# Kernel optimization log

Measured on AMD Instinct MI355X. Metric: run time of the kernel, lower is better.

The kernel has to match this reference:

```python
import jax, jax.numpy as jnp
import numpy as np

NF = 128                 # num_filters
C_STATE = NF * 3 // 2    # ODE state channels (output of conv_up_embed_1) = 192
EPS = 1e-5               # InstanceNorm2d eps
N_STEPS = 4              # fixed-step RK4 steps over t in [0, 1]
DT = 1.0 / N_STEPS

nl = jax.nn.softplus     # get_nonlinearity('softplus')


def instance_norm(x):
    # InstanceNorm2d(affine=False): normalize over (H, W) per (N, C)
    m = x.mean(axis=(2, 3), keepdims=True)
    v = x.var(axis=(2, 3), keepdims=True)
    return (x - m) * jax.lax.rsqrt(v + EPS)


def conv2d(x, w, b):
    y = jax.lax.conv_general_dilated(
        x, w, window_strides=(1, 1), padding='SAME',
        dimension_numbers=('NCHW', 'OIHW', 'NCHW'))
    return y + b[None, :, None, None]


def setup_inputs() -> dict:
    key = jax.random.key(0)
    ks = jax.random.split(key, 10)
    B, H, W = 4, 64, 64
    s = 0.05
    return {
        'x':    jax.random.normal(ks[0], (B, NF, H, W), jnp.float32),
        'skip': jax.random.normal(ks[1], (B, NF, 2 * H, 2 * W), jnp.float32),
        # InitialVelocity: 3x3 conv nf -> nf
        'iv_w': jax.random.normal(ks[2], (NF, NF, 3, 3), jnp.float32) * s,
        'iv_b': jax.random.normal(ks[3], (NF,), jnp.float32) * s,
        # conv_up_embed_1: 1x1 conv 3nf -> 3nf//2
        'up_w': jax.random.normal(ks[4], (C_STATE, 3 * NF, 1, 1), jnp.float32) * s,
        'up_b': jax.random.normal(ks[5], (C_STATE,), jnp.float32) * s,
        # ConvSODEFunc convs (second-order: dv/dt = f(z, v))
        'f1_w': jax.random.normal(ks[6], (C_STATE // 2, C_STATE, 3, 3), jnp.float32) * s,
        'f1_b': jax.random.normal(ks[7], (C_STATE // 2,), jnp.float32) * s,
        'f2_w': jax.random.normal(ks[8], (C_STATE // 2, C_STATE // 2, 3, 3), jnp.float32) * s,
        'f2_b': jax.random.normal(ks[9], (C_STATE // 2,), jnp.float32) * s,
    }


def _ode_f(y, f1_w, f1_b, f2_w, f2_b):
    # second-order ODE: state y = [z, v]; dz/dt = v, dv/dt = f(y)
    c = y.shape[1] // 2
    v = y[:, c:]
    u = nl(conv2d(instance_norm(y), f1_w, f1_b))   # [B, C/2, H, W]
    dv = nl(conv2d(instance_norm(u), f2_w, f2_b))  # [B, C/2, H, W]
    return jnp.concatenate([v, dv], axis=1)


def reference(x, skip, iv_w, iv_b, up_w, up_b, f1_w, f1_b, f2_w, f2_b):
    # InitialVelocity (counter == 0): concat learned velocity -> 2*nf channels
    v0 = nl(conv2d(instance_norm(x), iv_w, iv_b))
    y = jnp.concatenate([x, v0], axis=1)                       # [B, 2nf, H, W]
    B, C, H, W = y.shape
    # bilinear upsample x2, align_corners=False (half-pixel centers)
    y = jax.image.resize(y, (B, C, 2 * H, 2 * W), method='bilinear')
    y = jnp.concatenate([y, skip], axis=1)                     # [B, 3nf, 2H, 2W]
    y = nl(conv2d(y, up_w, up_b))                              # [B, 3nf//2, 2H, 2W]
    # ODEBlock: integrate t: 0 -> 1, fixed-step RK4 via lax.scan
    f = lambda s: _ode_f(s, f1_w, f1_b, f2_w, f2_b)

    def step(s, _):
        k1 = f(s)
        k2 = f(s + 0.5 * DT * k1)
        k3 = f(s + 0.5 * DT * k2)
        k4 = f(s + DT * k3)
        s = s + (DT / 6.0) * (k1 + 2.0 * k2 + 2.0 * k3 + k4)
        return s, None

    y, _ = jax.lax.scan(step, y, None, length=N_STEPS)
    return y
```

## Files before the change

### kernel.cpp

```cpp
#include <hip/hip_runtime.h>
#include <math.h>

#define BB 4
#define NF 128
#define CS 192
#define CH 96
#define H1 64
#define W1 64
#define H2 128
#define W2 128
#define P1 (H1*W1)
#define P2 (H2*W2)
#define EPSV 1e-5f
#define DTV 0.25f
#define NSLICE 32
#define SLOTSZ (1536 * NSLICE)

typedef __attribute__((ext_vector_type(8))) short short8;
typedef __attribute__((ext_vector_type(4))) float f32x4;

__device__ __forceinline__ float softplus_f(float x) {
    return fmaxf(x, 0.0f) + __logf(1.0f + __expf(-fabsf(x)));
}
__device__ __forceinline__ unsigned f2bf(float f) {
    unsigned u = __float_as_uint(f);
    return (u + 0x7FFFu + ((u >> 16) & 1u)) >> 16;
}
__device__ __forceinline__ float bf2f(short s) {
    return __uint_as_float(((unsigned)(unsigned short)s) << 16);
}
__device__ __forceinline__ int packbf(float a, float b) {
    return (int)(f2bf(a) | (f2bf(b) << 16));
}

__global__ __launch_bounds__(256) void zero_kernel(float* __restrict__ p, int n) {
    int i = blockIdx.x * 256 + threadIdx.x;
    if (i < n) p[i] = 0.f;
}

__global__ __launch_bounds__(256) void meanvar_raw_kernel(const float* __restrict__ x,
                                                          float* __restrict__ mv, int HW) {
    int bc = blockIdx.x;
    const float* p = x + (size_t)bc * HW;
    float s = 0.f, s2 = 0.f;
    for (int i = threadIdx.x; i < HW; i += 256) {
        float v = p[i];
        s += v; s2 += v * v;
    }
    __shared__ float sh[512];
    sh[threadIdx.x] = s; sh[256 + threadIdx.x] = s2;
    __syncthreads();
    for (int o = 128; o > 0; o >>= 1) {
        if (threadIdx.x < o) {
            sh[threadIdx.x] += sh[threadIdx.x + o];
            sh[256 + threadIdx.x] += sh[256 + threadIdx.x + o];
        }
        __syncthreads();
    }
    if (threadIdx.x == 0) {
        mv[2 * bc]     = sh[0];
        mv[2 * bc + 1] = sh[256];
    }
}

__global__ __launch_bounds__(256) void repack_w_kernel(const float* __restrict__ w,
                                                       short* __restrict__ wq,
                                                       int Cout, int Cin) {
    int idx = blockIdx.x * 256 + threadIdx.x;
    int total = Cout * Cin * 9;
    if (idx >= total) return;
    int tap = idx % 9;
    int t = idx / 9;
    int ci = t % Cin, co = t / Cin;
    int NITl = Cin >> 5, COGl = Cout >> 4;
    int cog = co >> 4, lx = co & 15;
    int it = ci >> 5, q = (ci >> 3) & 3, e = ci & 7;
    size_t o = ((((size_t)tap * NITl + it) * COGl + cog) * 64 + q * 16 + lx) * 8 + e;
    wq[o] = (short)f2bf(w[idx]);
}

__global__ __launch_bounds__(256) void repack_w1_kernel(const float* __restrict__ w,
                                                        short* __restrict__ wq, int n) {
    int i = blockIdx.x * 256 + threadIdx.x;
    if (i < n) wq[i] = (short)f2bf(w[i]);
}

__global__ __launch_bounds__(256) void xcvt_kernel(const float* __restrict__ x,
                                                   short* __restrict__ xbf) {
    __shared__ int buf[64 * 68];
    const int tid = threadIdx.x;
    const int px = tid & 63, jj = tid >> 6;
    const int px0 = blockIdx.x * 64;
    const int b = blockIdx.y;
#pragma unroll
    for (int ji = 0; ji < 16; ji++) {
        int j = jj + 4 * ji;
        int c = 2 * j;
        float a = x[((size_t)(b * NF + c)) * P1 + px0 + px];
        float d = x[((size_t)(b * NF + c + 1)) * P1 + px0 + px];
        buf[px * 68 + j] = packbf(a, d);
    }
    __syncthreads();
#pragma unroll
    for (int k = 0; k < 4; k++) {
        int idx = tid + 256 * k;
        int p2 = idx >> 4, w4 = idx & 15;
        int4 v = *(const int4*)&buf[p2 * 68 + w4 * 4];
        *(int4*)(xbf + ((size_t)b * P1 + px0 + p2) * NF + w4 * 8) = v;
    }
}

template<int CIN, int NCG, bool OUTBF, bool SUMS>
__global__ __launch_bounds__(512) void conv3x3_mfma(
    const short* __restrict__ in, const float* __restrict__ mvsums,
    const short* __restrict__ wq, const float* __restrict__ bias,
    float* __restrict__ outf, short* __restrict__ outbf, float* __restrict__ osum,
    int CoutT, int H, int W, int outC, int outCoff, int coblk)
{
    constexpr int ROWS = CIN + 8;
    constexpr int STGI = 180 * ROWS / 2;
    constexpr int SMEMI = (OUTBF && 128 * 52 > STGI) ? 128 * 52 : STGI;
    constexpr int NCGH = NCG / 2;
    __shared__ int smem[SMEMI];
    short* xt = (short*)smem;
    __shared__ float mvm[CIN], mvr[CIN];
    __shared__ float shs[2 * CH];
    const int tid = threadIdx.x;
    const int w8 = tid >> 6, lane = tid & 63;
    const int wy = w8 & 3, wc = w8 >> 2;
    const int lx = lane & 15, q = lane >> 4;
    const int x0 = blockIdx.x * 16, y0 = blockIdx.y * 8;
    const int b = blockIdx.z / coblk;
    const int co_base = (blockIdx.z % coblk) * (NCG * 16);
    const int slice = (blockIdx.x + (blockIdx.y << 3)) & (NSLICE - 1);
    const int HWp = H * W;
    const short* inb = in + (size_t)b * HWp * CIN;

    const float invHW = 1.0f / (float)HWp;
    for (int c = tid; c < CIN; c += 512) {
        float s = 0.f, s2 = 0.f;
#pragma unroll
        for (int sl = 0; sl < NSLICE; sl++) {
            s  += mvsums[(size_t)sl * 1536 + (b * CIN + c) * 2];
            s2 += mvsums[(size_t)sl * 1536 + (b * CIN + c) * 2 + 1];
        }
        float m  = s * invHW;
        float var = fmaxf(s2 * invHW - m * m, 0.f);
        mvm[c] = m;
        mvr[c] = rsqrtf(var + EPSV);
    }
    if (SUMS) for (int c = tid; c < 2 * CH; c += 512) shs[c] = 0.f;
    __syncthreads();

    constexpr int PARTS = CIN / 8;
    constexpr int TOT = 180 * PARTS;
    constexpr int NJ = (TOT + 511) / 512;
#pragma unroll
    for (int k = 0; k < NJ; k++) {
        int j = tid + 512 * k;
        if (j < TOT) {
            int px = j / PARTS, part = j - px * PARTS;
            int yy = px / 18, xx = px - yy * 18;
            int gy = y0 + yy - 1, gx = x0 + xx - 1;
            int4 wv = make_int4(0, 0, 0, 0);
            if (gy >= 0 && gy < H && gx >= 0 && gx < W) {
                int cb = part * 8;
                short8 v = *(const short8*)(inb + (size_t)(gy * W + gx) * CIN + cb);
                float4 m0 = *(const float4*)&mvm[cb];
                float4 m1 = *(const float4*)&mvm[cb + 4];
                float4 r0 = *(const float4*)&mvr[cb];
                float4 r1 = *(const float4*)&mvr[cb + 4];
                wv.x = packbf((bf2f(v[0]) - m0.x) * r0.x, (bf2f(v[1]) - m0.y) * r0.y);
                wv.y = packbf((bf2f(v[2]) - m0.z) * r0.z, (bf2f(v[3]) - m0.w) * r0.w);
                wv.z = packbf((bf2f(v[4]) - m1.x) * r1.x, (bf2f(v[5]) - m1.y) * r1.y);
                wv.w = packbf((bf2f(v[6]) - m1.z) * r1.z, (bf2f(v[7]) - m1.w) * r1.w);
            }
            *(int4*)(&xt[px * ROWS + part * 8]) = wv;
        }
    }
    __syncthreads();

    f32x4 acc[2][NCGH];
#pragma unroll
    for (int rr = 0; rr < 2; rr++)
#pragma unroll
        for (int cg = 0; cg < NCGH; cg++) acc[rr][cg] = (f32x4)(0.f);

    constexpr int NIT = CIN / 32;
    const int COGl = CoutT >> 4;
    const short* wbase = wq + ((size_t)((co_base >> 4) + wc * NCGH) * 64 + lane) * 8;
#pragma unroll 2
    for (int it = 0; it < NIT; it++) {
#pragma unroll
        for (int tap = 0; tap < 9; tap++) {
            const int dy = tap / 3, dx = tap % 3;
            const int slot0 = (tap * NIT + it) * COGl;
            short8 a[NCGH];
#pragma unroll
            for (int cg = 0; cg < NCGH; cg++)
                a[cg] = *(const short8*)(wbase + (size_t)(slot0 + cg) * 512);
#pragma unroll
            for (int rr = 0; rr < 2; rr++) {
                int row = wy * 2 + rr;
                short8 bfr = *(const short8*)(
                    &xt[((row + dy) * 18 + lx + dx) * ROWS + it * 32 + q * 8]);
#pragma unroll
                for (int cg = 0; cg < NCGH; cg++)
                    acc[rr][cg] = __builtin_amdgcn_mfma_f32_16x16x32_bf16(
                        a[cg], bfr, acc[rr][cg], 0, 0, 0);
            }
        }
    }

    if (OUTBF) __syncthreads();

    float s1l[NCGH][4], s2l[NCGH][4];
    if (SUMS) {
#pragma unroll
        for (int cg = 0; cg < NCGH; cg++)
#pragma unroll
            for (int r = 0; r < 4; r++) { s1l[cg][r] = 0.f; s2l[cg][r] = 0.f; }
    }
#pragma unroll
    for (int rr = 0; rr < 2; rr++) {
        int y = y0 + wy * 2 + rr;
#pragma unroll
        for (int cg = 0; cg < NCGH; cg++) {
            float v[4];
#pragma unroll
            for (int r = 0; r < 4; r++) {
                int co = wc * (NCGH * 16) + cg * 16 + q * 4 + r;
                v[r] = softplus_f(acc[rr][cg][r] + bias[co_base + co]);
                if (SUMS) { s1l[cg][r] += v[r]; s2l[cg][r] += v[r] * v[r]; }
            }
            if (OUTBF) {
                int pl = (wy * 2 + rr) * 16 + lx;
                smem[pl * 52 + wc * (NCGH * 8) + cg * 8 + q * 2]     = packbf(v[0], v[1]);
                smem[pl * 52 + wc * (NCGH * 8) + cg * 8 + q * 2 + 1] = packbf(v[2], v[3]);
            } else {
                float* ob = outf + ((size_t)b * outC + outCoff + co_base) * HWp
                            + y * W + x0 + lx;
#pragma unroll
                for (int r = 0; r < 4; r++)
                    ob[(size_t)(wc * (NCGH * 16) + cg * 16 + q * 4 + r) * HWp] = v[r];
            }
        }
    }
    if (OUTBF) {
        __syncthreads();
#pragma unroll
        for (int k = 0; k < 3; k++) {
            int idx = tid + 512 * k;
            int pl2 = idx / 12, w4 = idx % 12;
            int4 v = *(const int4*)&smem[pl2 * 52 + w4 * 4];
            int pix = (y0 + (pl2 >> 4)) * W + x0 + (pl2 & 15);
            *(int4*)(outbf + ((size_t)b * HWp + pix) * 96 + w4 * 8) = v;
        }
    }
    if (SUMS) {
#pragma unroll
        for (int cg = 0; cg < NCGH; cg++)
#pragma unroll
            for (int r = 0; r < 4; r++) {
                float a1 = s1l[cg][r], a2 = s2l[cg][r];
#pragma unroll
                for (int mask = 1; mask < 16; mask <<= 1) {
                    a1 += __shfl_xor(a1, mask);
                    a2 += __shfl_xor(a2, mask);
                }
                if (lx == 0) {
                    int co = wc * (NCGH * 16) + cg * 16 + q * 4 + r;
                    atomicAdd(&shs[2 * co], a1);
                    atomicAdd(&shs[2 * co + 1], a2);
                }
            }
        __syncthreads();
        for (int c = tid; c < 2 * NCG * 16; c += 512)
            atomicAdd(&osum[(size_t)slice * 1536 + (size_t)b * 2 * NCG * 16 + c], shs[c]);
    }
}

__global__ __launch_bounds__(256) void upsample_kernel(
    const float* __restrict__ x, const float* __restrict__ v0,
    const float* __restrict__ skip, short* __restrict__ ycat)
{
    __shared__ int buf[64 * 196];
    const int tid = threadIdx.x;
    const int px = tid & 63, jj = tid >> 6;
    const int px0 = blockIdx.x * 64;
    const int b = blockIdx.y;
    const int pxg = px0 + px;
    const int ox = pxg & 127, oy = pxg >> 7;
    int my = oy >> 1, mx = ox >> 1;
    int iy0 = (oy & 1) ? my : my - 1;
    float wy0 = (oy & 1) ? 0.75f : 0.25f;
    int ix0 = (ox & 1) ? mx : mx - 1;
    float wx0 = (ox & 1) ? 0.75f : 0.25f;
    int iy1 = min(iy0 + 1, H1 - 1); iy0 = max(iy0, 0);
    int ix1 = min(ix0 + 1, W1 - 1); ix0 = max(ix0, 0);
    float wy1 = 1.f - wy0, wx1 = 1.f - wx0;
    float w00 = wy0 * wx0, w01 = wy0 * wx1, w10 = wy1 * wx0, w11 = wy1 * wx1;
    int o00 = iy0 * W1 + ix0, o01 = iy0 * W1 + ix1;
    int o10 = iy1 * W1 + ix0, o11 = iy1 * W1 + ix1;
#pragma unroll 4
    for (int ji = 0; ji < 48; ji++) {
        int j = jj + 4 * ji;
        int c = 2 * j;
        float a, d;
        if (c < 256) {
            const float* s0 = (c < 128) ? x + ((size_t)(b * NF + c)) * P1
                                        : v0 + ((size_t)(b * NF + c - 128)) * P1;
            const float* s1 = s0 + P1;
            a = w00 * s0[o00] + w01 * s0[o01] + w10 * s0[o10] + w11 * s0[o11];
            d = w00 * s1[o00] + w01 * s1[o01] + w10 * s1[o10] + w11 * s1[o11];
        } else {
            const float* sk = skip + ((size_t)(b * NF + c - 256)) * P2 + pxg;
            a = sk[0]; d = sk[P2];
        }
        buf[px * 196 + j] = packbf(a, d);
    }
    __syncthreads();
#pragma unroll
    for (int k = 0; k < 12; k++) {
        int idx = tid + 256 * k;
        int p2 = idx / 48, w4 = idx % 48;
        int4 v = *(const int4*)&buf[p2 * 196 + w4 * 4];
        *(int4*)(ycat + ((size_t)b * P2 + px0 + p2) * 384 + w4 * 8) = v;
    }
}

__global__ __launch_bounds__(256) void conv1x1_mfma(
    const short* __restrict__ ycat, const short* __restrict__ wq,
    const float* __restrict__ bias, float* __restrict__ out,
    short* __restrict__ sbf, float* __restrict__ osum)
{
    __shared__ int smem[64 * 100];
    short* xs = (short*)smem;
    const int tid = threadIdx.x;
    const int wave = tid >> 6, lane = tid & 63;
    const int lx = lane & 15, q = lane >> 4;
    const int p0 = blockIdx.x * 64;
    const int b = blockIdx.y;
    const int slice = blockIdx.x & (NSLICE - 1);
    const int spx = tid >> 2, spart = tid & 3;
    const size_t gofs = ((size_t)b * P2 + p0 + spx) * 384 + spart * 8;
    const int ldso = spx * 40 + spart * 8;

    f32x4 acc[3][4];
#pragma unroll
    for (int cg = 0; cg < 3; cg++)
#pragma unroll
        for (int pg = 0; pg < 4; pg++) acc[cg][pg] = (f32x4)(0.f);

    short8 pf = *(const short8*)(ycat + gofs);
    for (int it = 0; it < 12; it++) {
        if (it > 0) __syncthreads();
        *(short8*)(&xs[ldso]) = pf;
        __syncthreads();
        if (it < 11) pf = *(const short8*)(ycat + gofs + (it + 1) * 32);
        const short* wl = wq + (size_t)(wave * 48 + lx) * 384 + it * 32 + q * 8;
        short8 a[3];
#pragma unroll
        for (int cg = 0; cg < 3; cg++)
            a[cg] = *(const short8*)(wl + (size_t)cg * 16 * 384);
#pragma unroll
        for (int pg = 0; pg < 4; pg++) {
            short8 bfr = *(const short8*)(&xs[(pg * 16 + lx) * 40 + q * 8]);
#pragma unroll
            for (int cg = 0; cg < 3; cg++)
                acc[cg][pg] = __builtin_amdgcn_mfma_f32_16x16x32_bf16(
                    a[cg], bfr, acc[cg][pg], 0, 0, 0);
        }
    }
    __syncthreads();

    float s1a[3][4], s2a[3][4];
#pragma unroll
    for (int cg = 0; cg < 3; cg++)
#pragma unroll
        for (int r = 0; r < 4; r++) { s1a[cg][r] = 0.f; s2a[cg][r] = 0.f; }
#pragma unroll
    for (int cg = 0; cg < 3; cg++) {
        int co0 = wave * 48 + cg * 16 + q * 4;
#pragma unroll
        for (int pg = 0; pg < 4; pg++) {
            int pl = pg * 16 + lx;
            float v[4];
#pragma unroll
            for (int r = 0; r < 4; r++) {
                v[r] = softplus_f(acc[cg][pg][r] + bias[co0 + r]);
                out[((size_t)(b * CS + co0 + r)) * P2 + p0 + pl] = v[r];
                s1a[cg][r] += v[r]; s2a[cg][r] += v[r] * v[r];
            }
            smem[pl * 100 + (co0 >> 1)]     = packbf(v[0], v[1]);
            smem[pl * 100 + (co0 >> 1) + 1] = packbf(v[2], v[3]);
        }
    }
    __syncthreads();
#pragma unroll
    for (int k = 0; k < 6; k++) {
        int idx = tid + 256 * k;
        int p2 = idx / 24, w4 = idx % 24;
        int4 v = *(const int4*)&smem[p2 * 100 + w4 * 4];
        *(int4*)(sbf + ((size_t)b * P2 + p0 + p2) * 192 + w4 * 8) = v;
    }
#pragma unroll
    for (int cg = 0; cg < 3; cg++)
#pragma unroll
        for (int r = 0; r < 4; r++) {
            float a1 = s1a[cg][r], a2 = s2a[cg][r];
#pragma unroll
            for (int mask = 1; mask < 16; mask <<= 1) {
                a1 += __shfl_xor(a1, mask);
                a2 += __shfl_xor(a2, mask);
            }
            if (lx == 0) {
                int co = wave * 48 + cg * 16 + q * 4 + r;
                atomicAdd(&osum[(size_t)slice * 1536 + ((size_t)b * CS + co) * 2], a1);
                atomicAdd(&osum[(size_t)slice * 1536 + ((size_t)b * CS + co) * 2 + 1], a2);
            }
        }
}

__global__ __launch_bounds__(256) void combine_kernel(
    const float* __restrict__ S, const float* __restrict__ Gx,
    const float* __restrict__ Gp, short* __restrict__ T, float* __restrict__ osum,
    float ca1, float ca2, float cb)
{
    __shared__ int buf[64 * 100];
    const int tid = threadIdx.x;
    const int px = tid & 63, jj = tid >> 6;
    const int px0 = blockIdx.x * 64;
    const int b = blockIdx.y;
    const int pxg = px0 + px;
    const int slice = blockIdx.x & (NSLICE - 1);
#pragma unroll 3
    for (int ji = 0; ji < 12; ji++) {
        int j = jj + 4 * ji;
        int c = 2 * j;
        size_t ia = ((size_t)(b * CS + c)) * P2 + pxg;
        size_t ib = ia + (size_t)CH * P2;
        size_t ig = ((size_t)(b * CH + c)) * P2 + pxg;
        float sa0 = S[ia], sa1 = S[ia + P2];
        float sb0 = S[ib], sb1 = S[ib + P2];
        float gx0 = Gx[ig], gx1 = Gx[ig + P2];
        float gp0 = Gp[ig], gp1 = Gp[ig + P2];
        buf[px * 100 + j]      = packbf(sa0 + ca1 * sb0 + ca2 * gx0,
                                        sa1 + ca1 * sb1 + ca2 * gx1);
        buf[px * 100 + 48 + j] = packbf(sb0 + cb * gp0, sb1 + cb * gp1);
    }
    __syncthreads();
#pragma unroll
    for (int k = 0; k < 6; k++) {
        int idx = tid + 256 * k;
        int p2 = idx / 24, w4 = idx % 24;
        int4 v = *(const int4*)&buf[p2 * 100 + w4 * 4];
        *(int4*)(T + ((size_t)b * P2 + px0 + p2) * 192 + w4 * 8) = v;
    }
    if (tid < 192) {
        int jj2 = tid >> 1, s = tid & 1;
        float s1lo = 0.f, s2lo = 0.f, s1hi = 0.f, s2hi = 0.f;
#pragma unroll 8
        for (int p = s; p < 64; p += 2) {
            int v = buf[p * 100 + jj2];
            float lo = bf2f((short)v), hi = bf2f((short)(v >> 16));
            s1lo += lo; s2lo += lo * lo; s1hi += hi; s2hi += hi * hi;
        }
        s1lo += __shfl_xor(s1lo, 1); s2lo += __shfl_xor(s2lo, 1);
        s1hi += __shfl_xor(s1hi, 1); s2hi += __shfl_xor(s2hi, 1);
        if (s == 0) {
            int c = 2 * jj2;
            float* dst = &osum[(size_t)slice * 1536 + ((size_t)b * CS + c) * 2];
            atomicAdd(dst, s1lo);
            atomicAdd(dst + 1, s2lo);
            atomicAdd(dst + 2, s1hi);
            atomicAdd(dst + 3, s2hi);
        }
    }
}

template<bool SBF>
__global__ __launch_bounds__(256) void final_kernel(
    float* __restrict__ S, const float* __restrict__ G1, const float* __restrict__ G2,
    const float* __restrict__ G3, const float* __restrict__ G4,
    short* __restrict__ sbf, float* __restrict__ osum)
{
    __shared__ int buf[SBF ? 64 * 100 : 4];
    const int tid = threadIdx.x;
    const int px = tid & 63, jj = tid >> 6;
    const int px0 = blockIdx.x * 64;
    const int b = blockIdx.y;
    const int pxg = px0 + px;
    const int slice = blockIdx.x & (NSLICE - 1);
    const float cA = DTV * DTV / 6.0f, cB = DTV / 6.0f;
#pragma unroll 3
    for (int ji = 0; ji < 12; ji++) {
        int j = jj + 4 * ji;
        int c = 2 * j;
        size_t ia = ((size_t)(b * CS + c)) * P2 + pxg;
        size_t ib = ia + (size_t)CH * P2;
        size_t ig = ((size_t)(b * CH + c)) * P2 + pxg;
        float sa0 = S[ia], sa1 = S[ia + P2];
        float sb0 = S[ib], sb1 = S[ib + P2];
        float g10 = G1[ig], g11 = G1[ig + P2];
        float g20 = G2[ig], g21 = G2[ig + P2];
        float g30 = G3[ig], g31 = G3[ig + P2];
        float g40 = G4[ig], g41 = G4[ig + P2];
        float na0 = sa0 + DTV * sb0 + cA * (g10 + g20 + g30);
        float na1 = sa1 + DTV * sb1 + cA * (g11 + g21 + g31);
        float nb0 = sb0 + cB * (g10 + 2.f * g20 + 2.f * g30 + g40);
        float nb1 = sb1 + cB * (g11 + 2.f * g21 + 2.f * g31 + g41);
        S[ia] = na0; S[ia + P2] = na1;
        S[ib] = nb0; S[ib + P2] = nb1;
        if (SBF) {
            buf[px * 100 + j]      = packbf(na0, na1);
            buf[px * 100 + 48 + j] = packbf(nb0, nb1);
        }
    }
    if (SBF) {
        __syncthreads();
#pragma unroll
        for (int k = 0; k < 6; k++) {
            int idx = tid + 256 * k;
            int p2 = idx / 24, w4 = idx % 24;
            int4 v = *(const int4*)&buf[p2 * 100 + w4 * 4];
            *(int4*)(sbf + ((size_t)b * P2 + px0 + p2) * 192 + w4 * 8) = v;
        }
        if (tid < 192) {
            int jj2 = tid >> 1, s = tid & 1;
            float s1lo = 0.f, s2lo = 0.f, s1hi = 0.f, s2hi = 0.f;
#pragma unroll 8
            for (int p = s; p < 64; p += 2) {
                int v = buf[p * 100 + jj2];
                float lo = bf2f((short)v), hi = bf2f((short)(v >> 16));
                s1lo += lo; s2lo += lo * lo; s1hi += hi; s2hi += hi * hi;
            }
            s1lo += __shfl_xor(s1lo, 1); s2lo += __shfl_xor(s2lo, 1);
            s1hi += __shfl_xor(s1hi, 1); s2hi += __shfl_xor(s2hi, 1);
            if (s == 0) {
                int c = 2 * jj2;
                float* dst = &osum[(size_t)slice * 1536 + ((size_t)b * CS + c) * 2];
                atomicAdd(dst, s1lo);
                atomicAdd(dst + 1, s2lo);
                atomicAdd(dst + 2, s1hi);
                atomicAdd(dst + 3, s2hi);
            }
        }
    }
}

extern "C" void kernel_launch(void* const* d_in, const int* in_sizes, int n_in,
                              void* d_out, int out_size, void* d_ws, size_t ws_size,
                              hipStream_t stream) {
    (void)in_sizes; (void)n_in; (void)out_size; (void)ws_size;
    const float* x    = (const float*)d_in[0];
    const float* skip = (const float*)d_in[1];
    const float* iv_w = (const float*)d_in[2];
    const float* iv_b = (const float*)d_in[3];
    const float* up_w = (const float*)d_in[4];
    const float* up_b = (const float*)d_in[5];
    const float* f1_w = (const float*)d_in[6];
    const float* f1_b = (const float*)d_in[7];
    const float* f2_w = (const float*)d_in[8];
    const float* f2_b = (const float*)d_in[9];

    float* S = (float*)d_out;
    float* ws = (float*)d_ws;
    const size_t NGf = (size_t)BB * CH * P2;
    float* G1 = ws;
    float* G2 = G1 + NGf;
    float* G3 = G2 + NGf;
    float* G4 = G3 + NGf;
    short* T   = (short*)(G4 + NGf);
    short* U   = T + (size_t)BB * P2 * CS;
    short* SBF = U + (size_t)BB * P2 * CH;
    float* MVS = (float*)(SBF + (size_t)BB * P2 * CS);
    short* IVQ = (short*)(MVS + (size_t)34 * SLOTSZ);
    short* F1Q = IVQ + (size_t)9 * NF * NF;
    short* F2Q = F1Q + (size_t)9 * CH * CS;
    short* UPQ = F2Q + (size_t)9 * CH * CH;
    short* YCAT = (short*)G1;
    float* V0   = G3;
    short* XBF  = (short*)G4;

    auto slot = [&](int i) { return MVS + (size_t)i * SLOTSZ; };

    zero_kernel<<<(34 * SLOTSZ + 255) / 256, 256, 0, stream>>>(MVS, 34 * SLOTSZ);
    repack_w_kernel<<<(NF * NF * 9 + 255) / 256, 256, 0, stream>>>(iv_w, IVQ, NF, NF);
    repack_w_kernel<<<(CH * CS * 9 + 255) / 256, 256, 0, stream>>>(f1_w, F1Q, CH, CS);
    repack_w_kernel<<<(CH * CH * 9 + 255) / 256, 256, 0, stream>>>(f2_w, F2Q, CH, CH);
    repack_w1_kernel<<<(CS * 384 + 255) / 256, 256, 0, stream>>>(up_w, UPQ, CS * 384);

    meanvar_raw_kernel<<<BB * NF, 256, 0, stream>>>(x, slot(0), P1);
    xcvt_kernel<<<dim3(P1 / 64, BB), 256, 0, stream>>>(x, XBF);
    conv3x3_mfma<128, 4, false, false><<<dim3(W1 / 16, H1 / 8, BB * 2), 512, 0, stream>>>(
        XBF, slot(0), IVQ, iv_b, V0, nullptr, nullptr, NF, H1, W1, NF, 0, 2);
    upsample_kernel<<<dim3(P2 / 64, BB), 256, 0, stream>>>(x, V0, skip, YCAT);
    conv1x1_mfma<<<dim3(P2 / 64, BB), 256, 0, stream>>>(YCAT, UPQ, up_b, S, SBF, slot(1));

    const float h = DTV;
    float* G[4] = {G1, G2, G3, G4};
    int sc = 2;
    float* yslot = slot(1);
    const dim3 egrd(P2 / 64, BB);

    for (int step = 0; step < 4; step++) {
        for (int sub = 0; sub < 4; sub++) {
            const short* Ybf = (sub == 0) ? SBF : T;
            float* uslot = slot(sc++);
            conv3x3_mfma<192, 6, true, true><<<dim3(W2 / 16, H2 / 8, BB), 512, 0, stream>>>(
                Ybf, yslot, F1Q, f1_b, nullptr, U, uslot, CH, H2, W2, CH, 0, 1);
            conv3x3_mfma<96, 6, false, false><<<dim3(W2 / 16, H2 / 8, BB), 512, 0, stream>>>(
                U, uslot, F2Q, f2_b, G[sub], nullptr, nullptr, CH, H2, W2, CH, 0, 1);
            if (sub < 3) {
                float ca1, ca2, cb;
                const float *Gx, *Gp;
                if (sub == 0)      { ca1 = h/2; ca2 = 0.f;     Gx = G1; Gp = G1; cb = h/2; }
                else if (sub == 1) { ca1 = h/2; ca2 = h*h/4;   Gx = G1; Gp = G2; cb = h/2; }
                else               { ca1 = h;   ca2 = h*h/2;   Gx = G2; Gp = G3; cb = h;   }
                float* tslot = slot(sc++);
                combine_kernel<<<egrd, 256, 0, stream>>>(S, Gx, Gp, T, tslot, ca1, ca2, cb);
                yslot = tslot;
            }
        }
        if (step < 3) {
            float* sslot = slot(sc++);
            final_kernel<true><<<egrd, 256, 0, stream>>>(S, G1, G2, G3, G4, SBF, sslot);
            yslot = sslot;
        } else {
            final_kernel<false><<<egrd, 256, 0, stream>>>(S, G1, G2, G3, G4, SBF, nullptr);
        }
    }
}
```

Baseline: 1.628 ms.

## Halve conv3x3 block to 4 waves with 4 rows each; stage full 1x1 input tile

The 3x3 conv kernel now runs 256 threads (4 waves) instead of 512. Each wave computes four output rows instead of two, so every weight fragment loaded from global memory feeds twice as many MFMAs. The 1x1 up-projection kernel now loads the whole 64-pixel by 384-channel tile into LDS once, replacing twelve synchronized chunk loads. Its weights are repacked into the MFMA fragment layout so each lane can read them contiguously. In exchange there are more accumulator registers per wave, fewer waves per block to hide latency, and larger LDS use in the 1x1 kernel.

```diff
diff --git a/kernel.cpp b/kernel.cpp
--- a/kernel.cpp
+++ b/kernel.cpp
@@ -80,9 +80,16 @@
 }
 
 __global__ __launch_bounds__(256) void repack_w1_kernel(const float* __restrict__ w,
-                                                        short* __restrict__ wq, int n) {
-    int i = blockIdx.x * 256 + threadIdx.x;
-    if (i < n) wq[i] = (short)f2bf(w[i]);
+                                                        short* __restrict__ wq,
+                                                        int Cout, int Cin) {
+    int idx = blockIdx.x * 256 + threadIdx.x;
+    if (idx >= Cout * Cin) return;
+    int ci = idx % Cin, co = idx / Cin;
+    int COGl = Cout >> 4;
+    int cog = co >> 4, lx = co & 15;
+    int it = ci >> 5, q = (ci >> 3) & 3, e = ci & 7;
+    size_t o = (((size_t)it * COGl + cog) * 64 + q * 16 + lx) * 8 + e;
+    wq[o] = (short)f2bf(w[idx]);
 }
 
 __global__ __launch_bounds__(256) void xcvt_kernel(const float* __restrict__ x,
@@ -111,7 +118,7 @@
 }
 
 template<int CIN, int NCG, bool OUTBF, bool SUMS>
-__global__ __launch_bounds__(512) void conv3x3_mfma(
+__global__ __launch_bounds__(256) void conv3x3_mfma(
     const short* __restrict__ in, const float* __restrict__ mvsums,
     const short* __restrict__ wq, const float* __restrict__ bias,
     float* __restrict__ outf, short* __restrict__ outbf, float* __restrict__ osum,
@@ -126,8 +133,8 @@
     __shared__ float mvm[CIN], mvr[CIN];
     __shared__ float shs[2 * CH];
     const int tid = threadIdx.x;
-    const int w8 = tid >> 6, lane = tid & 63;
-    const int wy = w8 & 3, wc = w8 >> 2;
+    const int w4 = tid >> 6, lane = tid & 63;
+    const int wy = w4 & 1, wc = w4 >> 1;
     const int lx = lane & 15, q = lane >> 4;
     const int x0 = blockIdx.x * 16, y0 = blockIdx.y * 8;
     const int b = blockIdx.z / coblk;
@@ -137,7 +144,7 @@
     const short* inb = in + (size_t)b * HWp * CIN;
 
     const float invHW = 1.0f / (float)HWp;
-    for (int c = tid; c < CIN; c += 512) {
+    for (int c = tid; c < CIN; c += 256) {
         float s = 0.f, s2 = 0.f;
 #pragma unroll
         for (int sl = 0; sl < NSLICE; sl++) {
@@ -149,15 +156,15 @@
         mvm[c] = m;
         mvr[c] = rsqrtf(var + EPSV);
     }
-    if (SUMS) for (int c = tid; c < 2 * CH; c += 512) shs[c] = 0.f;
+    if (SUMS) for (int c = tid; c < 2 * CH; c += 256) shs[c] = 0.f;
     __syncthreads();
 
     constexpr int PARTS = CIN / 8;
     constexpr int TOT = 180 * PARTS;
-    constexpr int NJ = (TOT + 511) / 512;
+    constexpr int NJ = (TOT + 255) / 256;
 #pragma unroll
     for (int k = 0; k < NJ; k++) {
-        int j = tid + 512 * k;
+        int j = tid + 256 * k;
         if (j < TOT) {
             int px = j / PARTS, part = j - px * PARTS;
             int yy = px / 18, xx = px - yy * 18;
@@ -180,9 +187,9 @@
     }
     __syncthreads();
 
-    f32x4 acc[2][NCGH];
-#pragma unroll
-    for (int rr = 0; rr < 2; rr++)
+    f32x4 acc[4][NCGH];
+#pragma unroll
+    for (int rr = 0; rr < 4; rr++)
 #pragma unroll
         for (int cg = 0; cg < NCGH; cg++) acc[rr][cg] = (f32x4)(0.f);
 
@@ -200,8 +207,8 @@
             for (int cg = 0; cg < NCGH; cg++)
                 a[cg] = *(const short8*)(wbase + (size_t)(slot0 + cg) * 512);
 #pragma unroll
-            for (int rr = 0; rr < 2; rr++) {
-                int row = wy * 2 + rr;
+            for (int rr = 0; rr < 4; rr++) {
+                int row = wy * 4 + rr;
                 short8 bfr = *(const short8*)(
                     &xt[((row + dy) * 18 + lx + dx) * ROWS + it * 32 + q * 8]);
 #pragma unroll
@@ -222,8 +229,8 @@
             for (int r = 0; r < 4; r++) { s1l[cg][r] = 0.f; s2l[cg][r] = 0.f; }
     }
 #pragma unroll
-    for (int rr = 0; rr < 2; rr++) {
-        int y = y0 + wy * 2 + rr;
+    for (int rr = 0; rr < 4; rr++) {
+        int y = y0 + wy * 4 + rr;
 #pragma unroll
         for (int cg = 0; cg < NCGH; cg++) {
             float v[4];
@@ -234,7 +241,7 @@
                 if (SUMS) { s1l[cg][r] += v[r]; s2l[cg][r] += v[r] * v[r]; }
             }
             if (OUTBF) {
-                int pl = (wy * 2 + rr) * 16 + lx;
+                int pl = (wy * 4 + rr) * 16 + lx;
                 smem[pl * 52 + wc * (NCGH * 8) + cg * 8 + q * 2]     = packbf(v[0], v[1]);
                 smem[pl * 52 + wc * (NCGH * 8) + cg * 8 + q * 2 + 1] = packbf(v[2], v[3]);
             } else {
@@ -249,12 +256,12 @@
     if (OUTBF) {
         __syncthreads();
 #pragma unroll
-        for (int k = 0; k < 3; k++) {
-            int idx = tid + 512 * k;
-            int pl2 = idx / 12, w4 = idx % 12;
-            int4 v = *(const int4*)&smem[pl2 * 52 + w4 * 4];
+        for (int k = 0; k < 6; k++) {
+            int idx = tid + 256 * k;
+            int pl2 = idx / 12, w4i = idx % 12;
+            int4 v = *(const int4*)&smem[pl2 * 52 + w4i * 4];
             int pix = (y0 + (pl2 >> 4)) * W + x0 + (pl2 & 15);
-            *(int4*)(outbf + ((size_t)b * HWp + pix) * 96 + w4 * 8) = v;
+            *(int4*)(outbf + ((size_t)b * HWp + pix) * 96 + w4i * 8) = v;
         }
     }
     if (SUMS) {
@@ -275,7 +282,7 @@
                 }
             }
         __syncthreads();
-        for (int c = tid; c < 2 * NCG * 16; c += 512)
+        for (int c = tid; c < 2 * NCG * 16; c += 256)
             atomicAdd(&osum[(size_t)slice * 1536 + (size_t)b * 2 * NCG * 16 + c], shs[c]);
     }
 }
@@ -334,7 +341,7 @@
     const float* __restrict__ bias, float* __restrict__ out,
     short* __restrict__ sbf, float* __restrict__ osum)
 {
-    __shared__ int smem[64 * 100];
+    __shared__ int smem[64 * 196];
     short* xs = (short*)smem;
     const int tid = threadIdx.x;
     const int wave = tid >> 6, lane = tid & 63;
@@ -342,9 +349,16 @@
     const int p0 = blockIdx.x * 64;
     const int b = blockIdx.y;
     const int slice = blockIdx.x & (NSLICE - 1);
-    const int spx = tid >> 2, spart = tid & 3;
-    const size_t gofs = ((size_t)b * P2 + p0 + spx) * 384 + spart * 8;
-    const int ldso = spx * 40 + spart * 8;
+
+    const short* yb = ycat + ((size_t)b * P2 + p0) * 384;
+#pragma unroll
+    for (int k = 0; k < 12; k++) {
+        int j = tid + 256 * k;
+        int spx = j / 48, spart = j - spx * 48;
+        short8 v = *(const short8*)(yb + (size_t)spx * 384 + spart * 8);
+        *(short8*)(&xs[spx * 392 + spart * 8]) = v;
+    }
+    __syncthreads();
 
     f32x4 acc[3][4];
 #pragma unroll
@@ -352,20 +366,16 @@
 #pragma unroll
         for (int pg = 0; pg < 4; pg++) acc[cg][pg] = (f32x4)(0.f);
 
-    short8 pf = *(const short8*)(ycat + gofs);
+    const short* wbase = wq + ((size_t)(wave * 3) * 64 + lane) * 8;
+#pragma unroll 2
     for (int it = 0; it < 12; it++) {
-        if (it > 0) __syncthreads();
-        *(short8*)(&xs[ldso]) = pf;
-        __syncthreads();
-        if (it < 11) pf = *(const short8*)(ycat + gofs + (it + 1) * 32);
-        const short* wl = wq + (size_t)(wave * 48 + lx) * 384 + it * 32 + q * 8;
         short8 a[3];
 #pragma unroll
         for (int cg = 0; cg < 3; cg++)
-            a[cg] = *(const short8*)(wl + (size_t)cg * 16 * 384);
+            a[cg] = *(const short8*)(wbase + (size_t)(it * 12 + cg) * 512);
 #pragma unroll
         for (int pg = 0; pg < 4; pg++) {
-            short8 bfr = *(const short8*)(&xs[(pg * 16 + lx) * 40 + q * 8]);
+            short8 bfr = *(const short8*)(&xs[(pg * 16 + lx) * 392 + it * 32 + q * 8]);
 #pragma unroll
             for (int cg = 0; cg < 3; cg++)
                 acc[cg][pg] = __builtin_amdgcn_mfma_f32_16x16x32_bf16(
@@ -589,11 +599,11 @@
     repack_w_kernel<<<(NF * NF * 9 + 255) / 256, 256, 0, stream>>>(iv_w, IVQ, NF, NF);
     repack_w_kernel<<<(CH * CS * 9 + 255) / 256, 256, 0, stream>>>(f1_w, F1Q, CH, CS);
     repack_w_kernel<<<(CH * CH * 9 + 255) / 256, 256, 0, stream>>>(f2_w, F2Q, CH, CH);
-    repack_w1_kernel<<<(CS * 384 + 255) / 256, 256, 0, stream>>>(up_w, UPQ, CS * 384);
+    repack_w1_kernel<<<(CS * 384 + 255) / 256, 256, 0, stream>>>(up_w, UPQ, CS, 384);
 
     meanvar_raw_kernel<<<BB * NF, 256, 0, stream>>>(x, slot(0), P1);
     xcvt_kernel<<<dim3(P1 / 64, BB), 256, 0, stream>>>(x, XBF);
-    conv3x3_mfma<128, 4, false, false><<<dim3(W1 / 16, H1 / 8, BB * 2), 512, 0, stream>>>(
+    conv3x3_mfma<128, 4, false, false><<<dim3(W1 / 16, H1 / 8, BB * 2), 256, 0, stream>>>(
         XBF, slot(0), IVQ, iv_b, V0, nullptr, nullptr, NF, H1, W1, NF, 0, 2);
     upsample_kernel<<<dim3(P2 / 64, BB), 256, 0, stream>>>(x, V0, skip, YCAT);
     conv1x1_mfma<<<dim3(P2 / 64, BB), 256, 0, stream>>>(YCAT, UPQ, up_b, S, SBF, slot(1));
@@ -608,9 +618,9 @@
         for (int sub = 0; sub < 4; sub++) {
             const short* Ybf = (sub == 0) ? SBF : T;
             float* uslot = slot(sc++);
-            conv3x3_mfma<192, 6, true, true><<<dim3(W2 / 16, H2 / 8, BB), 512, 0, stream>>>(
+            conv3x3_mfma<192, 6, true, true><<<dim3(W2 / 16, H2 / 8, BB), 256, 0, stream>>>(
                 Ybf, yslot, F1Q, f1_b, nullptr, U, uslot, CH, H2, W2, CH, 0, 1);
-            conv3x3_mfma<96, 6, false, false><<<dim3(W2 / 16, H2 / 8, BB), 512, 0, stream>>>(
+            conv3x3_mfma<96, 6, false, false><<<dim3(W2 / 16, H2 / 8, BB), 256, 0, stream>>>(
                 U, uslot, F2Q, f2_b, G[sub], nullptr, nullptr, CH, H2, W2, CH, 0, 1);
             if (sub < 3) {
                 float ca1, ca2, cb;
```

Result: slower. 1.675 ms (+2.9%).
